# Kernel optimization log

Hardware: AMD Instinct MI355X
Metric: run time of the kernel (lower is better)

Reference implementation:

```python
import jax, jax.numpy as jnp
import numpy as np

N = 50000      # num_nodes
E = 800000     # num_edges
D_IN = 128
D_HID = 128
D_EMB = 128
G = 4          # num_gcns
BN_EPS = 1e-5


def setup_inputs() -> dict:
    key = jax.random.key(0)
    ks = jax.random.split(key, 8)
    x = jax.random.normal(ks[0], (N, D_IN), dtype=jnp.float32)
    edge_index = jax.random.randint(ks[1], (2, E), 0, N, dtype=jnp.int64)
    # per-GCN params, stacked on leading G axis
    W1 = jax.random.normal(ks[2], (G, D_IN, D_HID), dtype=jnp.float32) / np.sqrt(D_IN)
    b1 = jnp.zeros((G, D_HID), dtype=jnp.float32)
    W2 = jax.random.normal(ks[3], (G, D_HID, D_EMB), dtype=jnp.float32) / np.sqrt(D_HID)
    b2 = jnp.zeros((G, D_EMB), dtype=jnp.float32)
    gamma1 = jnp.ones((G, D_HID), dtype=jnp.float32)
    beta1 = jnp.zeros((G, D_HID), dtype=jnp.float32)
    gamma2 = jnp.ones((G, D_EMB), dtype=jnp.float32)
    beta2 = jnp.zeros((G, D_EMB), dtype=jnp.float32)
    alpha = jnp.asarray(0.25, dtype=jnp.float32)  # PReLU (single shared param)
    mix_embed = jnp.full((N, G), 1.0 / G, dtype=jnp.float32)
    return {"x": x, "edge_index": edge_index, "W1": W1, "b1": b1, "W2": W2,
            "b2": b2, "gamma1": gamma1, "beta1": beta1, "gamma2": gamma2,
            "beta2": beta2, "alpha": alpha, "mix_embed": mix_embed}


def _gcn_norm(edge_index, num_nodes):
    # PyG GCNConv: add self-loops, symmetric normalization D^-1/2 (A+I) D^-1/2
    row, col = edge_index[0], edge_index[1]
    loop = jnp.arange(num_nodes, dtype=edge_index.dtype)
    row = jnp.concatenate([row, loop])
    col = jnp.concatenate([col, loop])
    w = jnp.ones(row.shape[0], dtype=jnp.float32)
    deg = jax.ops.segment_sum(w, col, num_segments=num_nodes)
    dinv = jnp.where(deg > 0, deg ** -0.5, 0.0)
    norm = dinv[row] * w * dinv[col]
    return row, col, norm


def _propagate(h, row, col, norm, num_nodes):
    # gather from source, scale by edge norm, scatter-add to target
    msg = h[row] * norm[:, None]
    return jax.ops.segment_sum(msg, col, num_segments=num_nodes)


def _batchnorm(z, gamma, beta):
    mu = jnp.mean(z, axis=0)
    var = jnp.mean((z - mu) ** 2, axis=0)  # biased, as torch BN training mode
    return (z - mu) * jax.lax.rsqrt(var + BN_EPS) * gamma + beta


def _prelu(z, alpha):
    return jnp.where(z > 0, z, alpha * z)


def reference(x, edge_index, W1, b1, W2, b2, gamma1, beta1, gamma2, beta2, alpha, mix_embed):
    num_nodes = x.shape[0]
    row, col, norm = _gcn_norm(edge_index, num_nodes)
    mix = jax.nn.softmax(mix_embed, axis=-1)  # [N, G]
    out = jnp.zeros((num_nodes, D_EMB), dtype=x.dtype)
    for g in range(G):  # small fixed number of mixture components
        h = x @ W1[g]
        z = _propagate(h, row, col, norm, num_nodes) + b1[g]
        z = _prelu(_batchnorm(z, gamma1[g], beta1[g]), alpha)
        h = z @ W2[g]
        z = _propagate(h, row, col, norm, num_nodes) + b2[g]
        z = _prelu(_batchnorm(z, gamma2[g], beta2[g]), alpha)
        out = out + mix[:, g:g + 1] * z
    return out
```

## Files before the change

kernel.cpp:

```cpp
#include <hip/hip_runtime.h>
#include <stdint.h>

static constexpr float EPS = 1e-5f;

typedef __attribute__((ext_vector_type(8))) short bfrag;
typedef __attribute__((ext_vector_type(4))) float ffrag;

__device__ __forceinline__ float bf2f(unsigned short u){
  union { unsigned int i; float f; } v; v.i = ((unsigned int)u) << 16; return v.f;
}
__device__ __forceinline__ unsigned short f2bf(float f){
  union { float f; unsigned int i; } v; v.f = f;
  unsigned int x = v.i;
  x += 0x7fffu + ((x >> 16) & 1u);
  return (unsigned short)(x >> 16);
}
__device__ __forceinline__ float lo16(unsigned int v){ return bf2f((unsigned short)(v & 0xffffu)); }
__device__ __forceinline__ float hi16(unsigned int v){ return bf2f((unsigned short)(v >> 16)); }
__device__ __forceinline__ unsigned int pack2(float a, float b){
  return ((unsigned int)f2bf(b) << 16) | (unsigned int)f2bf(a);
}

__global__ void k_deg(const int* __restrict__ col, int* __restrict__ indeg, int N, int E){
  int e = blockIdx.x * 256 + threadIdx.x;
  if (e < E){
    unsigned c = (unsigned)col[e];
    if (c < (unsigned)N) atomicAdd(&indeg[c], 1);
  }
}

__global__ void k_blocksum(const int* __restrict__ indeg, int* __restrict__ bsum, int N){
  __shared__ int sm[256];
  int i = blockIdx.x * 256 + threadIdx.x;
  sm[threadIdx.x] = (i < N) ? indeg[i] : 0;
  __syncthreads();
  for (int d = 128; d > 0; d >>= 1){
    if (threadIdx.x < d) sm[threadIdx.x] += sm[threadIdx.x + d];
    __syncthreads();
  }
  if (threadIdx.x == 0) bsum[blockIdx.x] = sm[0];
}

__global__ __launch_bounds__(1024) void k_scan_bsum(int* bsum, int nb){
  __shared__ int sm[1024];
  int t = threadIdx.x;
  int v = (t < nb) ? bsum[t] : 0;
  sm[t] = v;
  __syncthreads();
  for (int d = 1; d < 1024; d <<= 1){
    int u = (t >= d) ? sm[t - d] : 0;
    __syncthreads();
    sm[t] += u;
    __syncthreads();
  }
  if (t < nb) bsum[t] = sm[t] - v;
}

__global__ void k_scan_node(const int* __restrict__ indeg, const int* __restrict__ bsum,
                            int* __restrict__ offs, int* __restrict__ cursor,
                            float* __restrict__ dinv, int N){
  __shared__ int sm[256];
  int i = blockIdx.x * 256 + threadIdx.x;
  int v = (i < N) ? indeg[i] : 0;
  sm[threadIdx.x] = v;
  __syncthreads();
  for (int d = 1; d < 256; d <<= 1){
    int t = (threadIdx.x >= d) ? sm[threadIdx.x - d] : 0;
    __syncthreads();
    sm[threadIdx.x] += t;
    __syncthreads();
  }
  if (i < N){
    int o = bsum[blockIdx.x] + sm[threadIdx.x] - v;
    offs[i] = o; cursor[i] = o;
    dinv[i] = rsqrtf((float)(v + 1));
  }
}

__global__ void k_scatter(const int* __restrict__ row, const int* __restrict__ col,
                          int* __restrict__ cursor, int* __restrict__ csr, int N, int E){
  int e = blockIdx.x * 256 + threadIdx.x;
  if (e < E){
    unsigned c = (unsigned)col[e];
    if (c < (unsigned)N){
      int p = atomicAdd(&cursor[c], 1);
      unsigned r = (unsigned)row[e];
      csr[p] = (r < (unsigned)N) ? (int)r : 0;
    }
  }
}

__global__ void k_wcast(const float* __restrict__ W1, const float* __restrict__ W2,
                        unsigned short* __restrict__ Wt1, unsigned short* __restrict__ Wt2){
  int idx = blockIdx.x * 256 + threadIdx.x;
  const float* W = W1; unsigned short* Wt = Wt1;
  if (idx >= 65536){ idx -= 65536; W = W2; Wt = Wt2; }
  int c = idx >> 7, k = idx & 127;
  int g = c >> 7, j = c & 127;
  Wt[(size_t)c * 128 + k] = f2bf(W[(size_t)g*16384 + k*128 + j]);
}

__global__ void k_castx(const float* __restrict__ x, const float* __restrict__ dinv,
                        unsigned short* __restrict__ xs, int total4){
  int idx = blockIdx.x * 256 + threadIdx.x;
  int stride = gridDim.x * 256;
  for (; idx < total4; idx += stride){
    int i = idx >> 5;
    float di = dinv[i];
    float4 v = ((const float4*)x)[idx];
    ushort4 o;
    o.x = f2bf(di * v.x); o.y = f2bf(di * v.y);
    o.z = f2bf(di * v.z); o.w = f2bf(di * v.w);
    ((ushort4*)xs)[idx] = o;
  }
}

__global__ __launch_bounds__(256) void k_prop_x(const unsigned int* __restrict__ xs2,
                                               const int* __restrict__ csr,
                                               const int* __restrict__ offs, const int* __restrict__ indeg,
                                               const float* __restrict__ dinv,
                                               unsigned int* __restrict__ s2, int N){
  int i = blockIdx.x * 4 + (threadIdx.x >> 6);
  if (i >= N) return;
  int c2 = threadIdx.x & 63;
  unsigned int sv = xs2[(size_t)i*64 + c2];
  float ax = lo16(sv), ay = hi16(sv);
  int e = offs[i], end = e + indeg[i];
  for (; e + 8 <= end; e += 8){
    int r0 = csr[e], r1 = csr[e+1], r2 = csr[e+2], r3 = csr[e+3];
    int r4 = csr[e+4], r5 = csr[e+5], r6 = csr[e+6], r7 = csr[e+7];
    unsigned int v0 = xs2[(size_t)r0*64 + c2], v1 = xs2[(size_t)r1*64 + c2];
    unsigned int v2 = xs2[(size_t)r2*64 + c2], v3 = xs2[(size_t)r3*64 + c2];
    unsigned int v4 = xs2[(size_t)r4*64 + c2], v5 = xs2[(size_t)r5*64 + c2];
    unsigned int v6 = xs2[(size_t)r6*64 + c2], v7 = xs2[(size_t)r7*64 + c2];
    ax += lo16(v0)+lo16(v1)+lo16(v2)+lo16(v3)+lo16(v4)+lo16(v5)+lo16(v6)+lo16(v7);
    ay += hi16(v0)+hi16(v1)+hi16(v2)+hi16(v3)+hi16(v4)+hi16(v5)+hi16(v6)+hi16(v7);
  }
  for (; e < end; e++){
    unsigned int v = xs2[(size_t)csr[e]*64 + c2];
    ax += lo16(v); ay += hi16(v);
  }
  float di = dinv[i];
  s2[(size_t)i*64 + c2] = pack2(di * ax, di * ay);
}

__global__ __launch_bounds__(256) void k_gram(const unsigned short* __restrict__ in,
                                              int rstride, int coff128,
                                              float* __restrict__ Gbase, float* __restrict__ msumbase,
                                              int N){
  int gy = blockIdx.y;
  const unsigned short* src = in + gy * coff128;
  float* G = Gbase + (size_t)gy * 16384;
  float* msum = msumbase + gy * 128;

  __shared__ unsigned short st[128 * 40];
  __shared__ float colsum[128];

  int t = threadIdx.x;
  int wv = t >> 6, lane = t & 63, l16 = lane & 15, quad = lane >> 4;
  if (t < 128) colsum[t] = 0.f;

  int sn = t & 31, scb = t >> 5;

  ffrag acc[2][8];
  #pragma unroll
  for (int a = 0; a < 2; a++)
    #pragma unroll
    for (int b = 0; b < 8; b++) acc[a][b] = (ffrag){0.f,0.f,0.f,0.f};

  float cs[16];
  #pragma unroll
  for (int j = 0; j < 16; j++) cs[j] = 0.f;

  for (int c0 = blockIdx.x * 32; c0 < N; c0 += gridDim.x * 32){
    __syncthreads();
    int n = c0 + sn;
    ushort4 u0, u1, u2, u3;
    if (n < N){
      const ushort4* p = (const ushort4*)(src + (size_t)n * rstride + scb * 16);
      u0 = p[0]; u1 = p[1]; u2 = p[2]; u3 = p[3];
    } else {
      u0 = u1 = u2 = u3 = (ushort4){0,0,0,0};
    }
    unsigned short vals[16] = {u0.x,u0.y,u0.z,u0.w, u1.x,u1.y,u1.z,u1.w,
                               u2.x,u2.y,u2.z,u2.w, u3.x,u3.y,u3.z,u3.w};
    #pragma unroll
    for (int j = 0; j < 16; j++){
      st[(scb * 16 + j) * 40 + sn] = vals[j];
      cs[j] += bf2f(vals[j]);
    }
    __syncthreads();
    #pragma unroll
    for (int ta = 0; ta < 2; ta++){
      int ra = wv * 2 + ta;
      bfrag af = *(const bfrag*)&st[(ra * 16 + l16) * 40 + quad * 8];
      #pragma unroll
      for (int tb = 0; tb < 8; tb++){
        bfrag bf = *(const bfrag*)&st[(tb * 16 + l16) * 40 + quad * 8];
        acc[ta][tb] = __builtin_amdgcn_mfma_f32_16x16x32_bf16(af, bf, acc[ta][tb], 0, 0, 0);
      }
    }
  }
  #pragma unroll
  for (int j = 0; j < 16; j++) atomicAdd(&colsum[scb * 16 + j], cs[j]);
  __syncthreads();
  if (t < 128) atomicAdd(&msum[t], colsum[t]);
  #pragma unroll
  for (int ta = 0; ta < 2; ta++){
    #pragma unroll
    for (int tb = 0; tb < 8; tb++){
      int row0 = wv * 32 + ta * 16 + quad * 4;
      int colg = tb * 16 + l16;
      #pragma unroll
      for (int r = 0; r < 4; r++)
        atomicAdd(&G[(size_t)(row0 + r) * 128 + colg], acc[ta][tb][r]);
    }
  }
}

__global__ __launch_bounds__(64) void k_bnfit(const float* __restrict__ W,
                                              const float* __restrict__ gamma, const float* __restrict__ beta,
                                              const float* __restrict__ Gbase, int gmul,
                                              const float* __restrict__ msumbase, int mmul,
                                              float* __restrict__ scale, float* __restrict__ shiftF,
                                              float invN){
  int c = blockIdx.x;
  int g = c >> 7, j = c & 127;
  const float* Wc = W + (size_t)g * 16384 + j;
  const float* G  = Gbase + (size_t)g * gmul;
  const float* mv = msumbase + g * mmul;
  __shared__ float wl[128];
  __shared__ float ml[128];
  int t = threadIdx.x;
  for (int k = t; k < 128; k += 64){ wl[k] = Wc[(size_t)k * 128]; ml[k] = mv[k] * invN; }
  __syncthreads();
  float quad = 0.f, dm = 0.f;
  #pragma unroll
  for (int kk = 0; kk < 2; kk++){
    int k = t + kk * 64;
    float wk = wl[k];
    dm += ml[k] * wk;
    const float* Gr = G + (size_t)k * 128;
    float p = 0.f;
    for (int jj = 0; jj < 128; jj += 4){
      float4 gg = *(const float4*)(Gr + jj);
      float4 ww = *(const float4*)(wl + jj);
      p += gg.x*ww.x + gg.y*ww.y + gg.z*ww.z + gg.w*ww.w;
    }
    quad += wk * p;
  }
  for (int o = 32; o > 0; o >>= 1){
    quad += __shfl_down(quad, o);
    dm   += __shfl_down(dm, o);
  }
  if (t == 0){
    float var = quad * invN - dm * dm;
    float sc = gamma[c] * rsqrtf(var + EPS);
    scale[c] = sc;
    shiftF[c] = beta[c] - dm * sc;
  }
}

__global__ __launch_bounds__(256) void k_mm1f(const unsigned short* __restrict__ in,
                                              const unsigned short* __restrict__ Wt,
                                              const float* __restrict__ scale, const float* __restrict__ shiftF,
                                              const float* __restrict__ alpha_p, const float* __restrict__ dinv,
                                              unsigned short* __restrict__ h, int N){
  float alpha = alpha_p[0];
  int wave = threadIdx.x >> 6, lane = threadIdx.x & 63;
  int l16 = lane & 15, quad = lane >> 4;
  int node = blockIdx.x * 16 + l16;
  int nc = node < N ? node : N - 1;
  int colbase0 = wave * 128;
  float di = dinv[nc];

  const unsigned short* inrow = in + (size_t)nc * 128 + quad * 8;
  bfrag b0 = *(const bfrag*)(inrow);
  bfrag b1 = *(const bfrag*)(inrow + 32);
  bfrag b2 = *(const bfrag*)(inrow + 64);
  bfrag b3 = *(const bfrag*)(inrow + 96);

  #pragma unroll
  for (int ct = 0; ct < 8; ct++){
    int colbase = colbase0 + ct * 16;
    const unsigned short* wrow = Wt + (size_t)(colbase + l16) * 128 + quad * 8;
    bfrag a0 = *(const bfrag*)(wrow);
    bfrag a1 = *(const bfrag*)(wrow + 32);
    bfrag a2 = *(const bfrag*)(wrow + 64);
    bfrag a3 = *(const bfrag*)(wrow + 96);
    ffrag acc = {0.f, 0.f, 0.f, 0.f};
    acc = __builtin_amdgcn_mfma_f32_16x16x32_bf16(a0, b0, acc, 0, 0, 0);
    acc = __builtin_amdgcn_mfma_f32_16x16x32_bf16(a1, b1, acc, 0, 0, 0);
    acc = __builtin_amdgcn_mfma_f32_16x16x32_bf16(a2, b2, acc, 0, 0, 0);
    acc = __builtin_amdgcn_mfma_f32_16x16x32_bf16(a3, b3, acc, 0, 0, 0);
    int cb = colbase + quad * 4;
    float4 sc = *(const float4*)(scale + cb);
    float4 sh = *(const float4*)(shiftF + cb);
    float v0 = acc[0]*sc.x + sh.x; v0 = v0 > 0.f ? v0 : alpha*v0;
    float v1 = acc[1]*sc.y + sh.y; v1 = v1 > 0.f ? v1 : alpha*v1;
    float v2 = acc[2]*sc.z + sh.z; v2 = v2 > 0.f ? v2 : alpha*v2;
    float v3 = acc[3]*sc.w + sh.w; v3 = v3 > 0.f ? v3 : alpha*v3;
    uint2 o;
    o.x = pack2(di*v0, di*v1);
    o.y = pack2(di*v2, di*v3);
    if (node < N)
      *(uint2*)(h + (size_t)node * 512 + cb) = o;
  }
}

__global__ __launch_bounds__(256) void k_prop_h(const unsigned int* __restrict__ h2,
                                                const int* __restrict__ csr,
                                                const int* __restrict__ offs, const int* __restrict__ indeg,
                                                const float* __restrict__ dinv,
                                                unsigned int* __restrict__ t2, int N){
  int i = blockIdx.x;
  int c2 = threadIdx.x;
  unsigned int sv = h2[(size_t)i*256 + c2];
  float ax = lo16(sv), ay = hi16(sv);
  int e = offs[i], end = e + indeg[i];
  for (; e + 8 <= end; e += 8){
    int r0 = csr[e], r1 = csr[e+1], r2 = csr[e+2], r3 = csr[e+3];
    int r4 = csr[e+4], r5 = csr[e+5], r6 = csr[e+6], r7 = csr[e+7];
    unsigned int v0 = h2[(size_t)r0*256 + c2], v1 = h2[(size_t)r1*256 + c2];
    unsigned int v2 = h2[(size_t)r2*256 + c2], v3 = h2[(size_t)r3*256 + c2];
    unsigned int v4 = h2[(size_t)r4*256 + c2], v5 = h2[(size_t)r5*256 + c2];
    unsigned int v6 = h2[(size_t)r6*256 + c2], v7 = h2[(size_t)r7*256 + c2];
    ax += lo16(v0)+lo16(v1)+lo16(v2)+lo16(v3)+lo16(v4)+lo16(v5)+lo16(v6)+lo16(v7);
    ay += hi16(v0)+hi16(v1)+hi16(v2)+hi16(v3)+hi16(v4)+hi16(v5)+hi16(v6)+hi16(v7);
  }
  for (; e < end; e++){
    unsigned int v = h2[(size_t)csr[e]*256 + c2];
    ax += lo16(v); ay += hi16(v);
  }
  float di = dinv[i];
  t2[(size_t)i*256 + c2] = pack2(di * ax, di * ay);
}

__global__ __launch_bounds__(256) void k_mm2f(const unsigned short* __restrict__ t,
                                              const unsigned short* __restrict__ Wt,
                                              const float* __restrict__ scale, const float* __restrict__ shiftF,
                                              const float* __restrict__ alpha_p, const float* __restrict__ mixe,
                                              float* __restrict__ out, int N){
  __shared__ float red[4][16][132];
  float alpha = alpha_p[0];
  int wave = threadIdx.x >> 6, lane = threadIdx.x & 63;
  int l16 = lane & 15, quad = lane >> 4;
  int node = blockIdx.x * 16 + l16;
  int nc = node < N ? node : N - 1;

  float4 me = ((const float4*)mixe)[nc];
  float mx = fmaxf(fmaxf(me.x, me.y), fmaxf(me.z, me.w));
  float e0 = __expf(me.x - mx), e1 = __expf(me.y - mx), e2 = __expf(me.z - mx), e3 = __expf(me.w - mx);
  float inv = 1.f / (e0 + e1 + e2 + e3);
  float wvx = ((wave == 0) ? e0 : (wave == 1) ? e1 : (wave == 2) ? e2 : e3) * inv;

  const unsigned short* inrow = t + (size_t)nc * 512 + wave * 128 + quad * 8;
  bfrag b0 = *(const bfrag*)(inrow);
  bfrag b1 = *(const bfrag*)(inrow + 32);
  bfrag b2 = *(const bfrag*)(inrow + 64);
  bfrag b3 = *(const bfrag*)(inrow + 96);

  #pragma unroll
  for (int ct = 0; ct < 8; ct++){
    int c512 = wave * 128 + ct * 16;
    const unsigned short* wrow = Wt + (size_t)(c512 + l16) * 128 + quad * 8;
    bfrag a0 = *(const bfrag*)(wrow);
    bfrag a1 = *(const bfrag*)(wrow + 32);
    bfrag a2 = *(const bfrag*)(wrow + 64);
    bfrag a3 = *(const bfrag*)(wrow + 96);
    ffrag acc = {0.f, 0.f, 0.f, 0.f};
    acc = __builtin_amdgcn_mfma_f32_16x16x32_bf16(a0, b0, acc, 0, 0, 0);
    acc = __builtin_amdgcn_mfma_f32_16x16x32_bf16(a1, b1, acc, 0, 0, 0);
    acc = __builtin_amdgcn_mfma_f32_16x16x32_bf16(a2, b2, acc, 0, 0, 0);
    acc = __builtin_amdgcn_mfma_f32_16x16x32_bf16(a3, b3, acc, 0, 0, 0);
    int cb = c512 + quad * 4;
    float4 sc = *(const float4*)(scale + cb);
    float4 sh = *(const float4*)(shiftF + cb);
    float v0 = acc[0]*sc.x + sh.x; v0 = v0 > 0.f ? v0 : alpha*v0;
    float v1 = acc[1]*sc.y + sh.y; v1 = v1 > 0.f ? v1 : alpha*v1;
    float v2 = acc[2]*sc.z + sh.z; v2 = v2 > 0.f ? v2 : alpha*v2;
    float v3 = acc[3]*sc.w + sh.w; v3 = v3 > 0.f ? v3 : alpha*v3;
    int j = ct * 16 + quad * 4;
    float4 wr = {wvx*v0, wvx*v1, wvx*v2, wvx*v3};
    *(float4*)&red[wave][l16][j] = wr;
  }
  __syncthreads();
  int tt = threadIdx.x;
  int nn = tt >> 4, j0 = (tt & 15) * 8;
  int gnode = blockIdx.x * 16 + nn;
  if (gnode < N){
    float4 r0 = {0,0,0,0}, r1 = {0,0,0,0};
    #pragma unroll
    for (int w = 0; w < 4; w++){
      float4 p0 = *(const float4*)&red[w][nn][j0];
      float4 p1 = *(const float4*)&red[w][nn][j0 + 4];
      r0.x += p0.x; r0.y += p0.y; r0.z += p0.z; r0.w += p0.w;
      r1.x += p1.x; r1.y += p1.y; r1.z += p1.z; r1.w += p1.w;
    }
    float* op = out + (size_t)gnode * 128 + j0;
    *(float4*)(op) = r0;
    *(float4*)(op + 4) = r1;
  }
}

extern "C" void kernel_launch(void* const* d_in, const int* in_sizes, int n_in,
                              void* d_out, int out_size, void* d_ws, size_t ws_size,
                              hipStream_t stream) {
  const float* x      = (const float*)d_in[0];
  const int*   ei     = (const int*)d_in[1];
  const float* W1     = (const float*)d_in[2];
  const float* b1     = (const float*)d_in[3];
  const float* W2     = (const float*)d_in[4];
  const float* b2     = (const float*)d_in[5];
  const float* gamma1 = (const float*)d_in[6];
  const float* beta1  = (const float*)d_in[7];
  const float* gamma2 = (const float*)d_in[8];
  const float* beta2  = (const float*)d_in[9];
  const float* alpha  = (const float*)d_in[10];
  const float* mixe   = (const float*)d_in[11];
  float* out = (float*)d_out;
  (void)b1; (void)b2;

  const int N = in_sizes[0] / 128;
  const int E = in_sizes[1] / 2;
  const int* rowv = ei;
  const int* colv = ei + E;

  char* w = (char*)d_ws;
  size_t off = 0;
  auto take = [&](size_t bytes) -> void* {
    void* p = w + off;
    off = (off + bytes + 255) & ~(size_t)255;
    return p;
  };
  int*   indeg  = (int*)take((size_t)N * 4);
  int*   cursor = (int*)take((size_t)N * 4);
  int*   offs   = (int*)take((size_t)N * 4);
  int*   bsum   = (int*)take(4096);
  float* dinv   = (float*)take((size_t)N * 4);
  float* G1     = (float*)take(65536);
  float* G2     = (float*)take(262144);
  float* m1     = (float*)take(512);
  float* m2     = (float*)take(2048);
  float* scale1 = (float*)take(2048);
  float* shift1 = (float*)take(2048);
  float* scale2 = (float*)take(2048);
  float* shift2 = (float*)take(2048);
  int*   csr    = (int*)take((size_t)E * 4);
  unsigned short* Wt1 = (unsigned short*)take(512 * 128 * 2);
  unsigned short* Wt2 = (unsigned short*)take(512 * 128 * 2);
  unsigned short* xs = (unsigned short*)take((size_t)N * 128 * 2);
  unsigned short* sb = (unsigned short*)take((size_t)N * 128 * 2);
  unsigned short* h  = (unsigned short*)take((size_t)N * 512 * 2);
  unsigned short* tb = (unsigned short*)take((size_t)N * 512 * 2);

  hipMemsetAsync(indeg, 0, (size_t)N * 4, stream);
  hipMemsetAsync(G1, 0, 65536 + 262144 + 512 + 2048, stream);

  int ebl = (E + 255) / 256;
  int nb  = (N + 255) / 256;
  float invN = 1.0f / (float)N;

  k_deg<<<ebl, 256, 0, stream>>>(colv, indeg, N, E);
  k_blocksum<<<nb, 256, 0, stream>>>(indeg, bsum, N);
  k_scan_bsum<<<1, 1024, 0, stream>>>(bsum, nb);
  k_scan_node<<<nb, 256, 0, stream>>>(indeg, bsum, offs, cursor, dinv, N);
  k_scatter<<<ebl, 256, 0, stream>>>(rowv, colv, cursor, csr, N, E);

  k_wcast<<<512, 256, 0, stream>>>(W1, W2, Wt1, Wt2);
  k_castx<<<512, 256, 0, stream>>>(x, dinv, xs, N * 32);
  k_prop_x<<<(N + 3) / 4, 256, 0, stream>>>((const unsigned int*)xs, csr, offs, indeg, dinv, (unsigned int*)sb, N);

  k_gram<<<dim3(32, 1), 256, 0, stream>>>(sb, 128, 0, G1, m1, N);
  k_bnfit<<<512, 64, 0, stream>>>(W1, gamma1, beta1, G1, 0, m1, 0, scale1, shift1, invN);
  k_mm1f<<<(N + 15) / 16, 256, 0, stream>>>(sb, Wt1, scale1, shift1, alpha, dinv, h, N);

  k_prop_h<<<N, 256, 0, stream>>>((const unsigned int*)h, csr, offs, indeg, dinv, (unsigned int*)tb, N);

  k_gram<<<dim3(32, 4), 256, 0, stream>>>(tb, 512, 128, G2, m2, N);
  k_bnfit<<<512, 64, 0, stream>>>(W2, gamma2, beta2, G2, 16384, m2, 128, scale2, shift2, invN);
  k_mm2f<<<(N + 15) / 16, 256, 0, stream>>>(tb, Wt2, scale2, shift2, alpha, mixe, out, N);
}
```

Baseline: 600.9 us.

## Fuse CSR scan and prep kernels, merge memsets, remap prop_h threads

The three-kernel prefix scan is replaced by one kernel. Each wavefront does a shuffle scan of in-degrees and claims its base offset with an atomic on a global counter. The weight-cast and x-cast kernels are merged into one launch, and the two memsets become a single contiguous memset. k_prop_h now gives each block 8 nodes, with 32 threads each covering a 32-column slice, instead of one node per block. Together these cut launch count and small-kernel overhead. In exchange, the CSR neighbour order is no longer deterministic, and each gather touches narrower 128-byte segments.

```diff
diff --git a/kernel.cpp b/kernel.cpp
--- a/kernel.cpp
+++ b/kernel.cpp
@@ -29,51 +29,25 @@
   }
 }
 
-__global__ void k_blocksum(const int* __restrict__ indeg, int* __restrict__ bsum, int N){
-  __shared__ int sm[256];
-  int i = blockIdx.x * 256 + threadIdx.x;
-  sm[threadIdx.x] = (i < N) ? indeg[i] : 0;
-  __syncthreads();
-  for (int d = 128; d > 0; d >>= 1){
-    if (threadIdx.x < d) sm[threadIdx.x] += sm[threadIdx.x + d];
-    __syncthreads();
-  }
-  if (threadIdx.x == 0) bsum[blockIdx.x] = sm[0];
-}
-
-__global__ __launch_bounds__(1024) void k_scan_bsum(int* bsum, int nb){
-  __shared__ int sm[1024];
-  int t = threadIdx.x;
-  int v = (t < nb) ? bsum[t] : 0;
-  sm[t] = v;
-  __syncthreads();
-  for (int d = 1; d < 1024; d <<= 1){
-    int u = (t >= d) ? sm[t - d] : 0;
-    __syncthreads();
-    sm[t] += u;
-    __syncthreads();
-  }
-  if (t < nb) bsum[t] = sm[t] - v;
-}
-
-__global__ void k_scan_node(const int* __restrict__ indeg, const int* __restrict__ bsum,
-                            int* __restrict__ offs, int* __restrict__ cursor,
-                            float* __restrict__ dinv, int N){
-  __shared__ int sm[256];
-  int i = blockIdx.x * 256 + threadIdx.x;
-  int v = (i < N) ? indeg[i] : 0;
-  sm[threadIdx.x] = v;
-  __syncthreads();
-  for (int d = 1; d < 256; d <<= 1){
-    int t = (threadIdx.x >= d) ? sm[threadIdx.x - d] : 0;
-    __syncthreads();
-    sm[threadIdx.x] += t;
-    __syncthreads();
-  }
-  if (i < N){
-    int o = bsum[blockIdx.x] + sm[threadIdx.x] - v;
-    offs[i] = o; cursor[i] = o;
-    dinv[i] = rsqrtf((float)(v + 1));
+__global__ void k_alloc(const int* __restrict__ indeg, int* __restrict__ ctr,
+                        int* __restrict__ offs, int* __restrict__ cursor,
+                        float* __restrict__ dinv, int N){
+  int tid = blockIdx.x * 256 + threadIdx.x;
+  int lane = threadIdx.x & 63;
+  int v = (tid < N) ? indeg[tid] : 0;
+  int incl = v;
+  #pragma unroll
+  for (int d = 1; d < 64; d <<= 1){
+    int u = __shfl_up(incl, d);
+    if (lane >= d) incl += u;
+  }
+  int base = 0;
+  if (lane == 63) base = atomicAdd(ctr, incl);
+  base = __shfl(base, 63);
+  if (tid < N){
+    int o = base + incl - v;
+    offs[tid] = o; cursor[tid] = o;
+    dinv[tid] = rsqrtf((float)(v + 1));
   }
 }
 
@@ -90,28 +64,31 @@
   }
 }
 
-__global__ void k_wcast(const float* __restrict__ W1, const float* __restrict__ W2,
-                        unsigned short* __restrict__ Wt1, unsigned short* __restrict__ Wt2){
-  int idx = blockIdx.x * 256 + threadIdx.x;
-  const float* W = W1; unsigned short* Wt = Wt1;
-  if (idx >= 65536){ idx -= 65536; W = W2; Wt = Wt2; }
-  int c = idx >> 7, k = idx & 127;
-  int g = c >> 7, j = c & 127;
-  Wt[(size_t)c * 128 + k] = f2bf(W[(size_t)g*16384 + k*128 + j]);
-}
-
-__global__ void k_castx(const float* __restrict__ x, const float* __restrict__ dinv,
-                        unsigned short* __restrict__ xs, int total4){
-  int idx = blockIdx.x * 256 + threadIdx.x;
-  int stride = gridDim.x * 256;
-  for (; idx < total4; idx += stride){
-    int i = idx >> 5;
-    float di = dinv[i];
-    float4 v = ((const float4*)x)[idx];
-    ushort4 o;
-    o.x = f2bf(di * v.x); o.y = f2bf(di * v.y);
-    o.z = f2bf(di * v.z); o.w = f2bf(di * v.w);
-    ((ushort4*)xs)[idx] = o;
+__global__ void k_prep(const float* __restrict__ x, const float* __restrict__ dinv,
+                       unsigned short* __restrict__ xs,
+                       const float* __restrict__ W1, const float* __restrict__ W2,
+                       unsigned short* __restrict__ Wt1, unsigned short* __restrict__ Wt2,
+                       int total4x){
+  int b = blockIdx.x;
+  if (b < 512){
+    int idx = b * 256 + threadIdx.x;
+    const float* W = W1; unsigned short* Wt = Wt1;
+    if (idx >= 65536){ idx -= 65536; W = W2; Wt = Wt2; }
+    int c = idx >> 7, k = idx & 127;
+    int g = c >> 7, j = c & 127;
+    Wt[(size_t)c * 128 + k] = f2bf(W[(size_t)g*16384 + k*128 + j]);
+  } else {
+    int idx = (b - 512) * 256 + threadIdx.x;
+    int stride = (gridDim.x - 512) * 256;
+    for (; idx < total4x; idx += stride){
+      int i = idx >> 5;
+      float di = dinv[i];
+      float4 v = ((const float4*)x)[idx];
+      ushort4 o;
+      o.x = f2bf(di * v.x); o.y = f2bf(di * v.y);
+      o.z = f2bf(di * v.z); o.w = f2bf(di * v.w);
+      ((ushort4*)xs)[idx] = o;
+    }
   }
 }
 
@@ -313,8 +290,11 @@
                                                 const int* __restrict__ offs, const int* __restrict__ indeg,
                                                 const float* __restrict__ dinv,
                                                 unsigned int* __restrict__ t2, int N){
-  int i = blockIdx.x;
-  int c2 = threadIdx.x;
+  int B = blockIdx.x;
+  int s = B & 7, g = B >> 3;
+  int i = g * 8 + (threadIdx.x >> 5);
+  if (i >= N) return;
+  int c2 = s * 32 + (threadIdx.x & 31);
   unsigned int sv = h2[(size_t)i*256 + c2];
   float ax = lo16(sv), ay = hi16(sv);
   int e = offs[i], end = e + indeg[i];
@@ -409,9 +389,7 @@
   const float* x      = (const float*)d_in[0];
   const int*   ei     = (const int*)d_in[1];
   const float* W1     = (const float*)d_in[2];
-  const float* b1     = (const float*)d_in[3];
   const float* W2     = (const float*)d_in[4];
-  const float* b2     = (const float*)d_in[5];
   const float* gamma1 = (const float*)d_in[6];
   const float* beta1  = (const float*)d_in[7];
   const float* gamma2 = (const float*)d_in[8];
@@ -419,7 +397,6 @@
   const float* alpha  = (const float*)d_in[10];
   const float* mixe   = (const float*)d_in[11];
   float* out = (float*)d_out;
-  (void)b1; (void)b2;
 
   const int N = in_sizes[0] / 128;
   const int E = in_sizes[1] / 2;
@@ -433,15 +410,17 @@
     off = (off + bytes + 255) & ~(size_t)255;
     return p;
   };
+  size_t zbeg = off;
   int*   indeg  = (int*)take((size_t)N * 4);
-  int*   cursor = (int*)take((size_t)N * 4);
-  int*   offs   = (int*)take((size_t)N * 4);
-  int*   bsum   = (int*)take(4096);
-  float* dinv   = (float*)take((size_t)N * 4);
+  int*   ctr    = (int*)take(256);
   float* G1     = (float*)take(65536);
   float* G2     = (float*)take(262144);
   float* m1     = (float*)take(512);
   float* m2     = (float*)take(2048);
+  size_t zend = off;
+  int*   cursor = (int*)take((size_t)N * 4);
+  int*   offs   = (int*)take((size_t)N * 4);
+  float* dinv   = (float*)take((size_t)N * 4);
   float* scale1 = (float*)take(2048);
   float* shift1 = (float*)take(2048);
   float* scale2 = (float*)take(2048);
@@ -454,28 +433,24 @@
   unsigned short* h  = (unsigned short*)take((size_t)N * 512 * 2);
   unsigned short* tb = (unsigned short*)take((size_t)N * 512 * 2);
 
-  hipMemsetAsync(indeg, 0, (size_t)N * 4, stream);
-  hipMemsetAsync(G1, 0, 65536 + 262144 + 512 + 2048, stream);
+  hipMemsetAsync((char*)d_ws + zbeg, 0, zend - zbeg, stream);
 
   int ebl = (E + 255) / 256;
   int nb  = (N + 255) / 256;
   float invN = 1.0f / (float)N;
 
   k_deg<<<ebl, 256, 0, stream>>>(colv, indeg, N, E);
-  k_blocksum<<<nb, 256, 0, stream>>>(indeg, bsum, N);
-  k_scan_bsum<<<1, 1024, 0, stream>>>(bsum, nb);
-  k_scan_node<<<nb, 256, 0, stream>>>(indeg, bsum, offs, cursor, dinv, N);
+  k_alloc<<<nb, 256, 0, stream>>>(indeg, ctr, offs, cursor, dinv, N);
   k_scatter<<<ebl, 256, 0, stream>>>(rowv, colv, cursor, csr, N, E);
 
-  k_wcast<<<512, 256, 0, stream>>>(W1, W2, Wt1, Wt2);
-  k_castx<<<512, 256, 0, stream>>>(x, dinv, xs, N * 32);
+  k_prep<<<512 + 1024, 256, 0, stream>>>(x, dinv, xs, W1, W2, Wt1, Wt2, N * 32);
   k_prop_x<<<(N + 3) / 4, 256, 0, stream>>>((const unsigned int*)xs, csr, offs, indeg, dinv, (unsigned int*)sb, N);
 
   k_gram<<<dim3(32, 1), 256, 0, stream>>>(sb, 128, 0, G1, m1, N);
   k_bnfit<<<512, 64, 0, stream>>>(W1, gamma1, beta1, G1, 0, m1, 0, scale1, shift1, invN);
   k_mm1f<<<(N + 15) / 16, 256, 0, stream>>>(sb, Wt1, scale1, shift1, alpha, dinv, h, N);
 
-  k_prop_h<<<N, 256, 0, stream>>>((const unsigned int*)h, csr, offs, indeg, dinv, (unsigned int*)tb, N);
+  k_prop_h<<<((N + 7) / 8) * 8, 256, 0, stream>>>((const unsigned int*)h, csr, offs, indeg, dinv, (unsigned int*)tb, N);
 
   k_gram<<<dim3(32, 4), 256, 0, stream>>>(tb, 512, 128, G2, m2, N);
   k_bnfit<<<512, 64, 0, stream>>>(W2, gamma2, beta2, G2, 16384, m2, 128, scale2, shift2, invN);
```

After: 624.2 us. 1.04x slower.
